# Kernel tuning notes

Hardware: AMD Instinct MI355X
Metric: run time of the kernel (lower is better)

## Reference

```python
import jax, jax.numpy as jnp
import numpy as np

DIM = 1024
B, T = 4, 4096
CAP = 10.0
EPS_N = 1e-6
EPS_RMS = 1e-8


def softcap(x, a=CAP):
    return a * jnp.tanh(x / a)


def setup_inputs() -> dict:
    key = jax.random.key(0)
    k1, k2 = jax.random.split(key)
    x = jax.random.normal(k1, (B, T, DIM), dtype=jnp.float32)
    W = jax.random.normal(k2, (DIM, 4 * DIM), dtype=jnp.float32) / np.sqrt(DIM)
    b = jnp.zeros((4 * DIM,), dtype=jnp.float32)
    input_bias = -jnp.ones((DIM,), dtype=jnp.float32)  # Constant(-1.0) init
    scale = jnp.ones((DIM,), dtype=jnp.float32)        # RMSNorm scale
    return {"x": x, "W": W, "b": b, "input_bias": input_bias, "scale": scale}


def reference(x, W, b, input_bias, scale):
    # Batched projection once (the original recomputes Dense per step).
    pre = jnp.einsum('btd,df->btf', x, W) + b            # [B,T,4*dim]
    i_pre, f_pre, o_pre, z = jnp.split(pre, 4, axis=-1)  # each [B,T,dim]
    i_gate = softcap(i_pre + input_bias)                  # stabilized input gate pre-act
    f_gate = -jax.nn.softplus(f_pre)                      # log-forget gate
    o_sig = jax.nn.sigmoid(o_pre)
    tz = jnp.tanh(z)

    # Time-major for scan: [T,B,dim]
    seq = (jnp.swapaxes(i_gate, 0, 1), jnp.swapaxes(f_gate, 0, 1),
           jnp.swapaxes(o_sig, 0, 1), jnp.swapaxes(tz, 0, 1))

    c0 = jnp.zeros((x.shape[0], DIM), dtype=x.dtype)
    n0 = jnp.zeros_like(c0)
    m0 = jnp.zeros_like(c0)

    def step(carry, inp):
        c, n, m = carry
        i_t, f_t, o_t, tz_t = inp
        m_next = jnp.maximum(f_t + m, i_t)
        i_s = jnp.exp(i_t - m_next)
        f_s = jnp.exp(f_t + m - m_next)
        c = f_s * c + i_s * tz_t
        n = f_s * n + i_s
        h = o_t * (c / (n + EPS_N))
        return (c, n, m_next), h

    _, hs = jax.lax.scan(step, (c0, n0, m0), seq)  # hs: [T,B,dim]
    out = jnp.swapaxes(hs, 0, 1)                    # [B,T,dim]

    # RMSNorm
    rms = jnp.sqrt(jnp.mean(jnp.square(out), axis=-1, keepdims=True) + EPS_RMS)
    out = out / rms * scale
    # Dropout is identity at inference (training=False)
    return out
```

## Files before the change

kernel.cpp:

```cpp
#include <hip/hip_runtime.h>
#include <cstdint>
#include <cstddef>

#define TT    4096
#define NB    4
#define DIMV  1024
#define MTOT  (NB*TT)
#define KK    1024
#define NCOL  4096
#define NCH   64
#define CL    (TT/NCH)

#define BM 256
#define BN 256
#define BK 32


typedef _Float16 half4 __attribute__((ext_vector_type(4)));
typedef _Float16 half8 __attribute__((ext_vector_type(8)));
typedef float    f32x4 __attribute__((ext_vector_type(4)));
typedef __attribute__((address_space(1))) void GV;
typedef __attribute__((address_space(3))) void LV;

__device__ __forceinline__ void gload16(const void* g, void* l) {
    __builtin_amdgcn_global_load_lds((GV*)g, (LV*)l, 16, 0, 0);
}

__device__ __forceinline__ float ftanh(float x) {
    return 1.0f - 2.0f / (__expf(2.0f * x) + 1.0f);
}
__device__ __forceinline__ float fsig(float x) {
    return 1.0f / (1.0f + __expf(-x));
}
__device__ __forceinline__ float fsoftplus(float x) {
    return fmaxf(x, 0.0f) + __logf(1.0f + __expf(-fabsf(x)));
}

__global__ __launch_bounds__(256) void k_cvt_x(const float* __restrict__ x,
                                               _Float16* __restrict__ Xs) {
    const size_t i = ((size_t)blockIdx.x * 256 + threadIdx.x) * 8;
    const float4 a = *(const float4*)&x[i];
    const float4 b = *(const float4*)&x[i + 4];
    half8 o;
    o[0] = (_Float16)a.x; o[1] = (_Float16)a.y;
    o[2] = (_Float16)a.z; o[3] = (_Float16)a.w;
    o[4] = (_Float16)b.x; o[5] = (_Float16)b.y;
    o[6] = (_Float16)b.z; o[7] = (_Float16)b.w;
    *(half8*)&Xs[i] = o;
}

__global__ __launch_bounds__(256) void k_cvt_w(const float* __restrict__ W,
                                               _Float16* __restrict__ Wt) {
    __shared__ float tile[32][33];
    int tx = threadIdx.x & 31, ty = threadIdx.x >> 5;
    int nb = blockIdx.x * 32, kb = blockIdx.y * 32;
#pragma unroll
    for (int j = 0; j < 32; j += 8)
        tile[ty + j][tx] = W[(size_t)(kb + ty + j) * NCOL + nb + tx];
    __syncthreads();
#pragma unroll
    for (int j = 0; j < 32; j += 8)
        Wt[(size_t)(nb + ty + j) * KK + kb + tx] = (_Float16)tile[tx][ty + j];
}

__global__ __launch_bounds__(512) void k_gemm_gates(
    const _Float16* __restrict__ Xs, const _Float16* __restrict__ Wt,
    const float* __restrict__ bias, const float* __restrict__ ibias,
    _Float16* __restrict__ gi, _Float16* __restrict__ gf,
    _Float16* __restrict__ go, _Float16* __restrict__ gtz)
{
    __shared__ __align__(16) _Float16 Al0[BM * BK];
    __shared__ __align__(16) _Float16 Al1[BM * BK];
    __shared__ __align__(16) _Float16 Bl0[BN * BK];
    __shared__ __align__(16) _Float16 Bl1[BN * BK];
    const int tid  = threadIdx.x;
    const int lane = tid & 63;
    const int wave = tid >> 6;

    const int nwg = 16 * 64;
    int id = blockIdx.y * 16 + blockIdx.x;
    id = (id & 7) * (nwg >> 3) + (id >> 3);
    const int m0 = (id / 16) * BM;
    const int n0 = (id % 16) * BN;
    const int wm = (wave >> 2) * 128;
    const int wn = (wave & 3) * 64;

    const int r0  = tid >> 2;
    const int swz = (tid & 3) ^ ((r0 >> 1) & 3);
    const _Float16* aSrc = Xs + (size_t)(m0 + r0) * KK + swz * 8;
    const _Float16* bSrc = Wt + (size_t)(n0 + r0) * KK + swz * 8;

    f32x4 acc[8][4] = {};
    const int lr = lane & 15;
    const int ps = ((lane >> 4) ^ ((lr >> 1) & 3)) * 8;

#define STAGE(SRC, BUF, kkc)                                               \
    gload16(SRC + (kkc), &BUF[tid * 8]);                                   \
    gload16(SRC + (size_t)128 * KK + (kkc), &BUF[tid * 8 + 4096]);

#define COMPUTE(ABUF, BBUF)                                                \
    {                                                                      \
        half8 af[8], bf[4];                                                \
        _Pragma("unroll")                                                  \
        for (int mi = 0; mi < 8; ++mi)                                     \
            af[mi] = *(const half8*)&ABUF[(wm + mi * 16 + lr) * BK + ps];  \
        _Pragma("unroll")                                                  \
        for (int nj = 0; nj < 4; ++nj)                                     \
            bf[nj] = *(const half8*)&BBUF[(wn + nj * 16 + lr) * BK + ps];  \
        __builtin_amdgcn_s_setprio(1);                                     \
        _Pragma("unroll")                                                  \
        for (int mi = 0; mi < 8; ++mi)                                     \
            _Pragma("unroll")                                              \
            for (int nj = 0; nj < 4; ++nj)                                 \
                acc[mi][nj] = __builtin_amdgcn_mfma_f32_16x16x32_f16(      \
                    af[mi], bf[nj], acc[mi][nj], 0, 0, 0);                 \
        __builtin_amdgcn_s_setprio(0);                                     \
    }

    STAGE(aSrc, Al0, 0) STAGE(bSrc, Bl0, 0)
    __syncthreads();
#pragma unroll 1
    for (int t = 0; t < 15; ++t) {
        const int k1 = (2 * t + 1) * BK, k2 = (2 * t + 2) * BK;
        STAGE(aSrc, Al1, k1) STAGE(bSrc, Bl1, k1)
        COMPUTE(Al0, Bl0)
        __syncthreads();
        STAGE(aSrc, Al0, k2) STAGE(bSrc, Bl0, k2)
        COMPUTE(Al1, Bl1)
        __syncthreads();
    }
    {
        const int k1 = 31 * BK;
        STAGE(aSrc, Al1, k1) STAGE(bSrc, Bl1, k1)
        COMPUTE(Al0, Bl0)
        __syncthreads();
        COMPUTE(Al1, Bl1)
    }
#undef STAGE
#undef COMPUTE

    const int gate = n0 >> 10;
#pragma unroll
    for (int mi = 0; mi < 8; ++mi) {
        const int rowb  = m0 + wm + mi * 16 + (lane >> 4) * 4;
        const int abase = (rowb >> 3) * 8192 + (rowb & 7);
#pragma unroll
        for (int nj = 0; nj < 4; ++nj) {
            const int col = n0 + wn + nj * 16 + lr;
            const int d   = col & 1023;
            const float bb = bias[col];
            float v[4];
#pragma unroll
            for (int r = 0; r < 4; ++r) v[r] = acc[mi][nj][r] + bb;
            half4 o;
            if (gate == 0) {
                const float ib = ibias[d];
#pragma unroll
                for (int r = 0; r < 4; ++r)
                    o[r] = (_Float16)(10.0f * ftanh((v[r] + ib) * 0.1f));
                *(half4*)&gi[abase + d * 8] = o;
            } else if (gate == 1) {
#pragma unroll
                for (int r = 0; r < 4; ++r)
                    o[r] = (_Float16)(-fsoftplus(v[r]));
                *(half4*)&gf[abase + d * 8] = o;
            } else if (gate == 2) {
#pragma unroll
                for (int r = 0; r < 4; ++r)
                    o[r] = (_Float16)fsig(v[r]);
                *(half4*)&go[abase + d * 8] = o;
            } else {
#pragma unroll
                for (int r = 0; r < 4; ++r)
                    o[r] = (_Float16)ftanh(v[r]);
                *(half4*)&gtz[abase + d * 8] = o;
            }
        }
    }
}

__global__ __launch_bounds__(256) void k_scan1(
    const _Float16* __restrict__ gi, const _Float16* __restrict__ gf,
    const _Float16* __restrict__ gtz, float4* __restrict__ sums)
{
    const int ch = blockIdx.x * 256 + threadIdx.x;
    const int chunk = blockIdx.y;
    const int b = ch >> 10, d = ch & 1023;
    size_t base = (size_t)(b * 512 + chunk * 8) * 8192 + d * 8;
    float m = -1e30f, c = 0.0f, n = 0.0f, F = 0.0f;
#pragma unroll 2
    for (int t8 = 0; t8 < 8; ++t8, base += 8192) {
        const half8 i8 = *(const half8*)&gi[base];
        const half8 f8 = *(const half8*)&gf[base];
        const half8 z8 = *(const half8*)&gtz[base];
#pragma unroll
        for (int j = 0; j < 8; ++j) {
            const float iv = (float)i8[j];
            const float fv = (float)f8[j];
            const float zv = (float)z8[j];
            F += fv;
            const float mn = fmaxf(fv + m, iv);
            const float sc = __expf(fv + m - mn);
            const float si = __expf(iv - mn);
            c = sc * c + si * zv;
            n = sc * n + si;
            m = mn;
        }
    }
    sums[chunk * 4096 + ch] = make_float4(F, m, c, n);
}

__global__ __launch_bounds__(256) void k_scan2(const float4* __restrict__ sums,
                                               float4* __restrict__ states) {
    const int ch = blockIdx.x * 256 + threadIdx.x;
    float m = -1e30f, c = 0.0f, n = 0.0f;
    for (int chunk = 0; chunk < NCH; ++chunk) {
        states[chunk * 4096 + ch] = make_float4(m, c, n, 0.0f);
        const float4 s = sums[chunk * 4096 + ch];
        const float mn = fmaxf(m + s.x, s.y);
        const float e1 = __expf(m + s.x - mn);
        const float e2 = __expf(s.y - mn);
        c = e1 * c + e2 * s.z;
        n = e1 * n + e2 * s.w;
        m = mn;
    }
}

__global__ __launch_bounds__(256) void k_scan3(
    const _Float16* __restrict__ gi, const _Float16* __restrict__ gf,
    const _Float16* __restrict__ go, const _Float16* __restrict__ gtz,
    const float4* __restrict__ states, _Float16* __restrict__ hbuf)
{
    const int ch = blockIdx.x * 256 + threadIdx.x;
    const int chunk = blockIdx.y;
    const int b = ch >> 10, d = ch & 1023;
    size_t base = (size_t)(b * 512 + chunk * 8) * 8192 + d * 8;
    const float4 st = states[chunk * 4096 + ch];
    float m = st.x, c = st.y, n = st.z;
#pragma unroll 2
    for (int t8 = 0; t8 < 8; ++t8, base += 8192) {
        const half8 i8 = *(const half8*)&gi[base];
        const half8 f8 = *(const half8*)&gf[base];
        const half8 o8 = *(const half8*)&go[base];
        const half8 z8 = *(const half8*)&gtz[base];
        half8 h8;
#pragma unroll
        for (int j = 0; j < 8; ++j) {
            const float iv = (float)i8[j];
            const float fv = (float)f8[j];
            const float ov = (float)o8[j];
            const float zv = (float)z8[j];
            const float mn = fmaxf(fv + m, iv);
            const float sc = __expf(fv + m - mn);
            const float si = __expf(iv - mn);
            c = sc * c + si * zv;
            n = sc * n + si;
            m = mn;
            h8[j] = (_Float16)(ov * c / (n + 1e-6f));
        }
        *(half8*)&hbuf[base] = h8;
    }
}

__global__ __launch_bounds__(256) void k_rmsnorm(const _Float16* __restrict__ h,
                                                 const float* __restrict__ scale,
                                                 float* __restrict__ out) {
    const int tb  = blockIdx.x;
    const int tid = threadIdx.x;
    const int wid = tid >> 6, lane = tid & 63;
    const int d0  = tid * 4;
    const size_t tbase = (size_t)tb * 8192;

    float hv[4][8];
    float s[8] = {0, 0, 0, 0, 0, 0, 0, 0};
#pragma unroll
    for (int q = 0; q < 4; ++q) {
        const half8 v = *(const half8*)&h[tbase + (size_t)(d0 + q) * 8];
#pragma unroll
        for (int j = 0; j < 8; ++j) {
            hv[q][j] = (float)v[j];
            s[j] += hv[q][j] * hv[q][j];
        }
    }
#pragma unroll
    for (int j = 0; j < 8; ++j)
#pragma unroll
        for (int off = 32; off > 0; off >>= 1)
            s[j] += __shfl_xor(s[j], off, 64);

    __shared__ float red[4][8];
    if (lane == 0) {
#pragma unroll
        for (int j = 0; j < 8; ++j) red[wid][j] = s[j];
    }
    __syncthreads();
    float inv[8];
#pragma unroll
    for (int j = 0; j < 8; ++j)
        inv[j] = rsqrtf((red[0][j] + red[1][j] + red[2][j] + red[3][j]) *
                        (1.0f / 1024.0f) + 1e-8f);

    const float4 sc = *(const float4*)&scale[d0];
#pragma unroll
    for (int j = 0; j < 8; ++j) {
        float4 o;
        o.x = hv[0][j] * inv[j] * sc.x;
        o.y = hv[1][j] * inv[j] * sc.y;
        o.z = hv[2][j] * inv[j] * sc.z;
        o.w = hv[3][j] * inv[j] * sc.w;
        *(float4*)&out[(size_t)(tb * 8 + j) * 1024 + d0] = o;
    }
}

extern "C" void kernel_launch(void* const* d_in, const int* in_sizes, int n_in,
                              void* d_out, int out_size, void* d_ws, size_t ws_size,
                              hipStream_t stream) {
    (void)in_sizes; (void)n_in; (void)out_size; (void)ws_size;
    const float* x     = (const float*)d_in[0];
    const float* W     = (const float*)d_in[1];
    const float* bias  = (const float*)d_in[2];
    const float* ibias = (const float*)d_in[3];
    const float* scale = (const float*)d_in[4];
    float* out = (float*)d_out;

    char* ws = (char*)d_ws;
    size_t off = 0;
    _Float16* Xs = (_Float16*)(ws + off); off += (size_t)MTOT * KK * 2;
    _Float16* Wt = (_Float16*)(ws + off); off += (size_t)NCOL * KK * 2;
    _Float16* gi = (_Float16*)(ws + off); off += (size_t)MTOT * DIMV * 2;
    _Float16* gf = (_Float16*)(ws + off); off += (size_t)MTOT * DIMV * 2;
    _Float16* go = (_Float16*)(ws + off); off += (size_t)MTOT * DIMV * 2;
    _Float16* gtz= (_Float16*)(ws + off); off += (size_t)MTOT * DIMV * 2;
    float4* sums   = (float4*)(ws + off); off += (size_t)NCH * 4096 * 16;
    float4* states = (float4*)(ws + off); off += (size_t)NCH * 4096 * 16;
    _Float16* hbuf = Xs;

    k_cvt_x<<<(MTOT * DIMV) / (256 * 8), 256, 0, stream>>>(x, Xs);
    k_cvt_w<<<dim3(NCOL / 32, KK / 32), 256, 0, stream>>>(W, Wt);
    k_gemm_gates<<<dim3(NCOL / BN, MTOT / BM), 512, 0, stream>>>(
        Xs, Wt, bias, ibias, gi, gf, go, gtz);
    k_scan1<<<dim3(16, NCH), 256, 0, stream>>>(gi, gf, gtz, sums);
    k_scan2<<<16, 256, 0, stream>>>(sums, states);
    k_scan3<<<dim3(16, NCH), 256, 0, stream>>>(gi, gf, go, gtz, states, hbuf);
    k_rmsnorm<<<MTOT / 8, 256, 0, stream>>>(hbuf, scale, out);
}
```

Before: 261.7 us.

## Fuse chunked scan output pass with RMSNorm to drop intermediate h buffer

Merges the final scan pass and the RMSNorm kernel into one kernel. Each block handles one batch and time chunk across all 1024 channels, so the row RMS can be reduced in-block per timestep. This removes the fp16 h buffer's write and re-read and one launch. In exchange the grid shrinks fourfold, each thread carries four channel recurrences, and a block barrier is added per 8-step group, which lowers parallelism and latency hiding.

```diff
diff --git a/kernel.cpp b/kernel.cpp
--- a/kernel.cpp
+++ b/kernel.cpp
@@ -226,89 +226,77 @@
     }
 }
 
-__global__ __launch_bounds__(256) void k_scan3(
+__global__ __launch_bounds__(256) void k_scan3norm(
     const _Float16* __restrict__ gi, const _Float16* __restrict__ gf,
     const _Float16* __restrict__ go, const _Float16* __restrict__ gtz,
-    const float4* __restrict__ states, _Float16* __restrict__ hbuf)
+    const float4* __restrict__ states, const float* __restrict__ scale,
+    float* __restrict__ out)
 {
-    const int ch = blockIdx.x * 256 + threadIdx.x;
+    const int b = blockIdx.x;
     const int chunk = blockIdx.y;
-    const int b = ch >> 10, d = ch & 1023;
-    size_t base = (size_t)(b * 512 + chunk * 8) * 8192 + d * 8;
-    const float4 st = states[chunk * 4096 + ch];
-    float m = st.x, c = st.y, n = st.z;
-#pragma unroll 2
-    for (int t8 = 0; t8 < 8; ++t8, base += 8192) {
-        const half8 i8 = *(const half8*)&gi[base];
-        const half8 f8 = *(const half8*)&gf[base];
-        const half8 o8 = *(const half8*)&go[base];
-        const half8 z8 = *(const half8*)&gtz[base];
-        half8 h8;
-#pragma unroll
-        for (int j = 0; j < 8; ++j) {
-            const float iv = (float)i8[j];
-            const float fv = (float)f8[j];
-            const float ov = (float)o8[j];
-            const float zv = (float)z8[j];
-            const float mn = fmaxf(fv + m, iv);
-            const float sc = __expf(fv + m - mn);
-            const float si = __expf(iv - mn);
-            c = sc * c + si * zv;
-            n = sc * n + si;
-            m = mn;
-            h8[j] = (_Float16)(ov * c / (n + 1e-6f));
-        }
-        *(half8*)&hbuf[base] = h8;
-    }
-}
-
-__global__ __launch_bounds__(256) void k_rmsnorm(const _Float16* __restrict__ h,
-                                                 const float* __restrict__ scale,
-                                                 float* __restrict__ out) {
-    const int tb  = blockIdx.x;
     const int tid = threadIdx.x;
     const int wid = tid >> 6, lane = tid & 63;
-    const int d0  = tid * 4;
-    const size_t tbase = (size_t)tb * 8192;
-
-    float hv[4][8];
-    float s[8] = {0, 0, 0, 0, 0, 0, 0, 0};
+    __shared__ float red[2][4][8];
+
+    float m[4], c[4], n[4], sv[4];
 #pragma unroll
     for (int q = 0; q < 4; ++q) {
-        const half8 v = *(const half8*)&h[tbase + (size_t)(d0 + q) * 8];
-#pragma unroll
-        for (int j = 0; j < 8; ++j) {
-            hv[q][j] = (float)v[j];
-            s[j] += hv[q][j] * hv[q][j];
+        const float4 st = states[chunk * 4096 + b * 1024 + tid + q * 256];
+        m[q] = st.x; c[q] = st.y; n[q] = st.z;
+        sv[q] = scale[tid + q * 256];
+    }
+
+    size_t base = (size_t)(b * 512 + chunk * 8) * 8192 + tid * 8;
+    const size_t obase0 = (size_t)(b * TT + chunk * CL) * DIMV + tid;
+#pragma unroll 1
+    for (int t8 = 0; t8 < 8; ++t8, base += 8192) {
+        float hv[4][8];
+        float s[8] = {0, 0, 0, 0, 0, 0, 0, 0};
+#pragma unroll
+        for (int q = 0; q < 4; ++q) {
+            const size_t qb = base + (size_t)q * 2048;
+            const half8 i8 = *(const half8*)&gi[qb];
+            const half8 f8 = *(const half8*)&gf[qb];
+            const half8 o8 = *(const half8*)&go[qb];
+            const half8 z8 = *(const half8*)&gtz[qb];
+#pragma unroll
+            for (int j = 0; j < 8; ++j) {
+                const float iv = (float)i8[j];
+                const float fv = (float)f8[j];
+                const float ov = (float)o8[j];
+                const float zv = (float)z8[j];
+                const float mn = fmaxf(fv + m[q], iv);
+                const float sc = __expf(fv + m[q] - mn);
+                const float si = __expf(iv - mn);
+                c[q] = sc * c[q] + si * zv;
+                n[q] = sc * n[q] + si;
+                m[q] = mn;
+                hv[q][j] = ov * c[q] / (n[q] + 1e-6f);
+                s[j] += hv[q][j] * hv[q][j];
+            }
         }
-    }
-#pragma unroll
-    for (int j = 0; j < 8; ++j)
-#pragma unroll
-        for (int off = 32; off > 0; off >>= 1)
-            s[j] += __shfl_xor(s[j], off, 64);
-
-    __shared__ float red[4][8];
-    if (lane == 0) {
-#pragma unroll
-        for (int j = 0; j < 8; ++j) red[wid][j] = s[j];
-    }
-    __syncthreads();
-    float inv[8];
-#pragma unroll
-    for (int j = 0; j < 8; ++j)
-        inv[j] = rsqrtf((red[0][j] + red[1][j] + red[2][j] + red[3][j]) *
-                        (1.0f / 1024.0f) + 1e-8f);
-
-    const float4 sc = *(const float4*)&scale[d0];
-#pragma unroll
-    for (int j = 0; j < 8; ++j) {
-        float4 o;
-        o.x = hv[0][j] * inv[j] * sc.x;
-        o.y = hv[1][j] * inv[j] * sc.y;
-        o.z = hv[2][j] * inv[j] * sc.z;
-        o.w = hv[3][j] * inv[j] * sc.w;
-        *(float4*)&out[(size_t)(tb * 8 + j) * 1024 + d0] = o;
+#pragma unroll
+        for (int j = 0; j < 8; ++j)
+#pragma unroll
+            for (int off = 32; off > 0; off >>= 1)
+                s[j] += __shfl_xor(s[j], off, 64);
+        if (lane == 0) {
+#pragma unroll
+            for (int j = 0; j < 8; ++j) red[t8 & 1][wid][j] = s[j];
+        }
+        __syncthreads();
+        float inv[8];
+#pragma unroll
+        for (int j = 0; j < 8; ++j)
+            inv[j] = rsqrtf((red[t8 & 1][0][j] + red[t8 & 1][1][j] +
+                             red[t8 & 1][2][j] + red[t8 & 1][3][j]) *
+                            (1.0f / 1024.0f) + 1e-8f);
+        const size_t ob = obase0 + (size_t)t8 * 8 * DIMV;
+#pragma unroll
+        for (int j = 0; j < 8; ++j)
+#pragma unroll
+            for (int q = 0; q < 4; ++q)
+                out[ob + (size_t)j * DIMV + q * 256] = hv[q][j] * inv[j] * sv[q];
     }
 }
 
@@ -333,7 +321,6 @@
     _Float16* gtz= (_Float16*)(ws + off); off += (size_t)MTOT * DIMV * 2;
     float4* sums   = (float4*)(ws + off); off += (size_t)NCH * 4096 * 16;
     float4* states = (float4*)(ws + off); off += (size_t)NCH * 4096 * 16;
-    _Float16* hbuf = Xs;
 
     k_cvt_x<<<(MTOT * DIMV) / (256 * 8), 256, 0, stream>>>(x, Xs);
     k_cvt_w<<<dim3(NCOL / 32, KK / 32), 256, 0, stream>>>(W, Wt);
@@ -341,6 +328,5 @@
         Xs, Wt, bias, ibias, gi, gf, go, gtz);
     k_scan1<<<dim3(16, NCH), 256, 0, stream>>>(gi, gf, gtz, sums);
     k_scan2<<<16, 256, 0, stream>>>(sums, states);
-    k_scan3<<<dim3(16, NCH), 256, 0, stream>>>(gi, gf, go, gtz, states, hbuf);
-    k_rmsnorm<<<MTOT / 8, 256, 0, stream>>>(hbuf, scale, out);
-}
+    k_scan3norm<<<dim3(NB, NCH), 256, 0, stream>>>(gi, gf, go, gtz, states, scale, out);
+}
```

New measurement: 264.2 us. Within noise of the previous version (+1.0%).
